# Optimization experiments

Hardware: AMD Instinct MI355X
Metric: run time of the kernel (lower is better)

Reference implementation:

```python
import jax, jax.numpy as jnp
import numpy as np

MAX_VALUATION = 5  # init kwarg
N = 4096           # == n_samples, so subsampling branch is skipped
D = 512
IDX_MAX = 200000


def setup_inputs() -> dict:
    key = jax.random.key(0)
    k1, k2 = jax.random.split(key)
    z = jax.random.normal(k1, (N, D), dtype=jnp.float32)
    indices = jax.random.randint(k2, (N,), 0, IDX_MAX, dtype=jnp.int64 if jax.config.jax_enable_x64 else jnp.int32)
    return {"z": z, "indices": indices}


def _pairwise_dist(z):
    # torch.cdist(z, z), p=2, with a sqrt-safe formulation
    sq = jnp.sum(z * z, axis=-1)                      # [n]
    d2 = sq[:, None] + sq[None, :] - 2.0 * (z @ z.T)  # [n, n]
    d2 = jnp.maximum(d2, 0.0)
    pos = d2 > 0.0
    return jnp.where(pos, jnp.sqrt(jnp.where(pos, d2, 1.0)), 0.0)


def _valuation_capped(diff, cap):
    # v3(diff) capped at `cap`: v >= t  <=>  diff % 3**t == 0 (for diff > 0)
    val = jnp.zeros(diff.shape, dtype=jnp.int32)
    for t in range(1, cap + 1):
        val = val + (diff % (3 ** t) == 0).astype(jnp.int32)
    return val


def reference(z, indices):
    n = z.shape[0]
    dist = _pairwise_dist(z)                               # [n, n]
    diff = jnp.abs(indices[:, None] - indices[None, :])    # [n, n] int
    # cap valuation at MAX_VALUATION+1 so over-cap pairs match no level v<=MAX_VALUATION
    val = _valuation_capped(diff, MAX_VALUATION + 1)
    upper = jnp.triu(jnp.ones((n, n), dtype=bool), k=1)
    valid = upper & (diff > 0)

    total = jnp.float32(0.0)
    level_count = jnp.float32(0.0)
    for v in range(MAX_VALUATION + 1):
        target = jnp.float32(3.0 ** (-v))
        weight = jnp.float32(1.0 / (v + 1))
        mask = valid & (val == v)
        cnt = jnp.sum(mask)
        sq = jnp.where(mask, (dist - target) ** 2, 0.0)
        mse = jnp.sum(sq) / jnp.maximum(cnt, 1).astype(jnp.float32)
        use = cnt >= 2  # original skips levels with <2 pairs
        total = total + jnp.where(use, weight * mse, 0.0)
        level_count = level_count + use.astype(jnp.float32)
    return total / jnp.maximum(level_count, 1.0)
```

## Files before the change

### kernel.cpp

```cpp
#include <hip/hip_runtime.h>
#include <hip/hip_bf16.h>
#include <stdint.h>

typedef unsigned short u16;
typedef unsigned int   u32;
typedef unsigned long long u64;

#define N_ROWS 4096
#define DIM    512
#define NT64   64
#define NPAIR64 2080
#define MOD3   729
#define NLEV   6
#define NKP    8
#define NSLOT  64

typedef __attribute__((ext_vector_type(2))) long  long2v;
typedef __attribute__((ext_vector_type(4))) float f32x4;

#define WS_ZPK 0
#define WS_SQ  (N_ROWS * DIM)
#define WS_R   (WS_SQ + N_ROWS * 4)
#define WS_ACC (WS_R + N_ROWS * 4)

__global__ __launch_bounds__(256)
void prep_kernel(const float* __restrict__ z, const int* __restrict__ idx,
                 u64* __restrict__ zpack, float* __restrict__ sq,
                 int* __restrict__ rres, u32* __restrict__ acczero)
{
    const int lane = threadIdx.x & 63;
    const int row  = blockIdx.x * 4 + (threadIdx.x >> 6);
    const float4* zr = reinterpret_cast<const float4*>(z + (size_t)row * DIM) + lane * 2;
    float4 v0 = zr[0], v1 = zr[1];
    float f[8] = {v0.x, v0.y, v0.z, v0.w, v1.x, v1.y, v1.z, v1.w};
    float ss = 0.f;
#pragma unroll
    for (int k = 0; k < 8; ++k) ss += f[k] * f[k];
    int lo = __builtin_amdgcn_cvt_pk_fp8_f32(f[0], f[1], 0, false);
    lo     = __builtin_amdgcn_cvt_pk_fp8_f32(f[2], f[3], lo, true);
    int hi = __builtin_amdgcn_cvt_pk_fp8_f32(f[4], f[5], 0, false);
    hi     = __builtin_amdgcn_cvt_pk_fp8_f32(f[6], f[7], hi, true);
    const u64 pk = (u64)(u32)lo | ((u64)(u32)hi << 32);
    zpack[((size_t)((row >> 4) * 8 + (lane >> 3)) << 7)
          + ((lane & 3) * 16 + (row & 15)) * 2 + ((lane >> 2) & 1)] = pk;
#pragma unroll
    for (int off = 32; off > 0; off >>= 1) ss += __shfl_down(ss, off, 64);
    if (lane == 0) {
        sq[row]   = ss;
        rres[row] = idx[row] % MOD3;
    }
    if (row == 0) {
#pragma unroll
        for (int i = 0; i < 16; ++i) acczero[lane + i * 64] = 0u;
    }
}

template<bool DIAG>
__device__ __forceinline__ void epilogue_acc(
    const f32x4 (&acc)[4][4], const float* sqI, const float* sqJ,
    const int* rI, const int* rJ, int lane,
    float (&lsum)[NLEV], u64& pcnt)
{
    const int rbase = (lane >> 4) * 4;
    const int cbase = lane & 15;
#pragma unroll
    for (int m = 0; m < 4; ++m) {
        const int il0 = m * 16 + rbase;
#pragma unroll
        for (int n = 0; n < 4; ++n) {
            const int jl  = n * 16 + cbase;
            const float sqj = sqJ[jl];
            const int   rj  = rJ[jl];
#pragma unroll
            for (int q = 0; q < 4; ++q) {
                const int il = il0 + q;
                float d2 = fmaxf(sqI[il] + sqj - 2.0f * acc[m][n][q], 0.f);
                const float dist = __builtin_amdgcn_sqrtf(d2);
                int dm = rI[il] - rj;
                dm += (dm >> 31) & MOD3;
                const u32 x = (u32)dm;
                int v =
                    (x * 2863311531u <= 1431655765u) +
                    (x *  954437177u <=  477218588u) +
                    (x * 1749801491u <=  159072862u) +
                    (x * 2014922929u <=   53024287u) +
                    (x * 3534952507u <=   17674762u) +
                    (x * 4041629033u <=    5891587u);
                if (DIAG) {
                    v = (jl > il) ? v : 6;
                }
                float tv = 1.0f;
                tv = (v == 1) ? (1.f / 3.f)   : tv;
                tv = (v == 2) ? (1.f / 9.f)   : tv;
                tv = (v == 3) ? (1.f / 27.f)  : tv;
                tv = (v == 4) ? (1.f / 81.f)  : tv;
                tv = (v == 5) ? (1.f / 243.f) : tv;
                const float dd  = dist - tv;
                const float sqd = dd * dd;
#pragma unroll
                for (int vv = 0; vv < NLEV; ++vv)
                    lsum[vv] += (v == vv) ? sqd : 0.f;
                pcnt += 1ull << (8 * v);
            }
        }
    }
}

__global__ __launch_bounds__(64, 2)
void pair_kernel(const u64* __restrict__ zpack, const float* __restrict__ sq,
                 const int* __restrict__ rres, float* __restrict__ gsum2,
                 u32* __restrict__ gcnt2)
{
    __shared__ __align__(16) u64 sb[2][8][128];
    __shared__ float sqI[64], sqJ[64];
    __shared__ int   rI[64], rJ[64];

    const int lane = threadIdx.x;

    const int wg = (blockIdx.x & 7) * (NPAIR64 / 8) + (blockIdx.x >> 3);
    int t = wg, ti = 0, rem = NT64;
    while (t >= rem) { t -= rem; ++ti; --rem; }
    const int tj = ti + t;
    const int I0 = ti * 64, J0 = tj * 64;

    __builtin_amdgcn_global_load_lds(
        (const __attribute__((address_space(1))) u32*)(sq + I0 + lane),
        (__attribute__((address_space(3))) u32*)sqI, 4, 0, 0);
    __builtin_amdgcn_global_load_lds(
        (const __attribute__((address_space(1))) u32*)(sq + J0 + lane),
        (__attribute__((address_space(3))) u32*)sqJ, 4, 0, 0);
    __builtin_amdgcn_global_load_lds(
        (const __attribute__((address_space(1))) u32*)(rres + I0 + lane),
        (__attribute__((address_space(3))) u32*)rI, 4, 0, 0);
    __builtin_amdgcn_global_load_lds(
        (const __attribute__((address_space(1))) u32*)(rres + J0 + lane),
        (__attribute__((address_space(3))) u32*)rJ, 4, 0, 0);

    const int RA = ti * 4, RB = tj * 4;

#define STAGE(buf, kp)                                                         \
    {                                                                          \
        _Pragma("unroll")                                                      \
        for (int g = 0; g < 4; ++g) {                                          \
            __builtin_amdgcn_global_load_lds(                                  \
                (const __attribute__((address_space(1))) u32*)                 \
                    (zpack + (((size_t)(RA + g) * 8 + (kp)) << 7) + lane * 2), \
                (__attribute__((address_space(3))) u32*)&sb[buf][g][0],        \
                16, 0, 0);                                                     \
            __builtin_amdgcn_global_load_lds(                                  \
                (const __attribute__((address_space(1))) u32*)                 \
                    (zpack + (((size_t)(RB + g) * 8 + (kp)) << 7) + lane * 2), \
                (__attribute__((address_space(3))) u32*)&sb[buf][4 + g][0],    \
                16, 0, 0);                                                     \
        }                                                                      \
    }

    f32x4 acc[4][4];
#pragma unroll
    for (int m = 0; m < 4; ++m)
#pragma unroll
        for (int n = 0; n < 4; ++n) acc[m][n] = (f32x4){0.f, 0.f, 0.f, 0.f};

    STAGE(0, 0);
#pragma unroll
    for (int kp = 0; kp < NKP; ++kp) {
        const int buf = kp & 1;
        if (kp + 1 < NKP) {
            STAGE(buf ^ 1, kp + 1);
            asm volatile("s_waitcnt vmcnt(8)" ::: "memory");
        } else {
            asm volatile("s_waitcnt vmcnt(0)" ::: "memory");
        }
        __builtin_amdgcn_sched_barrier(0);
        long2v A[4], B[4];
#pragma unroll
        for (int g = 0; g < 4; ++g) {
            A[g] = reinterpret_cast<const long2v*>(&sb[buf][g][0])[lane];
            B[g] = reinterpret_cast<const long2v*>(&sb[buf][4 + g][0])[lane];
        }
#pragma unroll
        for (int h = 0; h < 2; ++h)
#pragma unroll
            for (int m = 0; m < 4; ++m)
#pragma unroll
                for (int n = 0; n < 4; ++n)
                    acc[m][n] = __builtin_amdgcn_mfma_f32_16x16x32_fp8_fp8(
                        A[m][h], B[n][h], acc[m][n], 0, 0, 0);
    }
#undef STAGE

    float lsum[NLEV] = {0.f, 0.f, 0.f, 0.f, 0.f, 0.f};
    u64 pcnt = 0ull;
    if (ti == tj) epilogue_acc<true >(acc, sqI, sqJ, rI, rJ, lane, lsum, pcnt);
    else          epilogue_acc<false>(acc, sqI, sqJ, rI, rJ, lane, lsum, pcnt);

    const int slot = (int)(blockIdx.x & (NSLOT - 1));
#pragma unroll
    for (int vv = 0; vv < NLEV; ++vv) {
        float s = lsum[vv];
        u32   c = (u32)((pcnt >> (8 * vv)) & 255ull);
#pragma unroll
        for (int off = 32; off > 0; off >>= 1) {
            s += __shfl_xor(s, off, 64);
            c += __shfl_xor(c, off, 64);
        }
        if (lane == 0) {
            atomicAdd(&gsum2[slot * 8 + vv], s);
            atomicAdd(&gcnt2[slot * 8 + vv], c);
        }
    }
}

__global__ __launch_bounds__(64)
void finalize_kernel(const float* __restrict__ gsum2,
                     const u32* __restrict__ gcnt2,
                     float* __restrict__ out)
{
    const int lane = threadIdx.x;
    float s[NLEV];
    u32   c[NLEV];
#pragma unroll
    for (int v = 0; v < NLEV; ++v) {
        s[v] = gsum2[lane * 8 + v];
        c[v] = gcnt2[lane * 8 + v];
    }
#pragma unroll
    for (int v = 0; v < NLEV; ++v) {
#pragma unroll
        for (int off = 32; off > 0; off >>= 1) {
            s[v] += __shfl_xor(s[v], off, 64);
            c[v] += __shfl_xor(c[v], off, 64);
        }
    }
    if (lane == 0) {
        const float w[NLEV] = {1.f, 1.f / 2.f, 1.f / 3.f, 1.f / 4.f, 1.f / 5.f, 1.f / 6.f};
        float total = 0.f, lc = 0.f;
#pragma unroll
        for (int v = 0; v < NLEV; ++v) {
            const float cnt = (float)c[v];
            const float mse = s[v] / fmaxf(cnt, 1.f);
            const bool  use = c[v] >= 2u;
            total += use ? w[v] * mse : 0.f;
            lc    += use ? 1.f : 0.f;
        }
        out[0] = total / fmaxf(lc, 1.f);
    }
}

extern "C" void kernel_launch(void* const* d_in, const int* in_sizes, int n_in,
                              void* d_out, int out_size, void* d_ws, size_t ws_size,
                              hipStream_t stream)
{
    const float* z   = (const float*)d_in[0];
    const int*   idx = (const int*)d_in[1];
    char* ws = (char*)d_ws;
    u64*   zpk   = (u64*)(ws + WS_ZPK);
    float* sq    = (float*)(ws + WS_SQ);
    int*   rres  = (int*)(ws + WS_R);
    float* gsum2 = (float*)(ws + WS_ACC);
    u32*   gcnt2 = (u32*)(ws + WS_ACC + NSLOT * 8 * 4);
    float* out   = (float*)d_out;

    prep_kernel<<<N_ROWS / 4, 256, 0, stream>>>(z, idx, zpk, sq, rres, (u32*)gsum2);
    pair_kernel<<<NPAIR64, 64, 0, stream>>>(zpk, sq, rres, gsum2, gcnt2);
    finalize_kernel<<<1, 64, 0, stream>>>(gsum2, gcnt2, out);
}
```

Baseline: 37.39 us.

## Precompute per-level counts via residue histogram and use LUT weights in pair epilogue

A histogram of index residues mod 729 now gives the per-level pair counts in closed form. The per-level MSE weights are folded into a 729-entry coefficient/target lookup table, so the pair kernel accumulates a single weighted sum per pair instead of six sums plus packed counts. The pair tile also shrinks from 64x64 to 32x32, which gives four times as many workgroups and higher occupancy. The cost is an extra memset and a single-block count kernel, more redundant operand loads across smaller tiles, and LDS lookups with data-dependent addresses.

```diff
diff --git a/kernel.cpp b/kernel.cpp
--- a/kernel.cpp
+++ b/kernel.cpp
@@ -8,25 +8,29 @@
 
 #define N_ROWS 4096
 #define DIM    512
-#define NT64   64
-#define NPAIR64 2080
+#define NT32   128
+#define NPAIR32 8256
 #define MOD3   729
-#define NLEV   6
 #define NKP    8
 #define NSLOT  64
 
 typedef __attribute__((ext_vector_type(2))) long  long2v;
+typedef __attribute__((ext_vector_type(2))) float f32x2;
 typedef __attribute__((ext_vector_type(4))) float f32x4;
 
-#define WS_ZPK 0
-#define WS_SQ  (N_ROWS * DIM)
-#define WS_R   (WS_SQ + N_ROWS * 4)
-#define WS_ACC (WS_R + N_ROWS * 4)
+#define WS_ZPK  0
+#define WS_SQ   (N_ROWS * DIM)
+#define WS_R    (WS_SQ + N_ROWS * 4)
+#define WS_HIST (WS_R + N_ROWS * 4)
+#define WS_GS   (WS_HIST + 736 * 4)
+#define WS_META (WS_GS + 64 * 4)
+#define WS_LUTG (WS_META + 16)
+#define WS_ZERO_BYTES (736 * 4 + 64 * 4)
 
 __global__ __launch_bounds__(256)
 void prep_kernel(const float* __restrict__ z, const int* __restrict__ idx,
                  u64* __restrict__ zpack, float* __restrict__ sq,
-                 int* __restrict__ rres, u32* __restrict__ acczero)
+                 int* __restrict__ rres, u32* __restrict__ hist)
 {
     const int lane = threadIdx.x & 63;
     const int row  = blockIdx.x * 4 + (threadIdx.x >> 6);
@@ -46,102 +50,143 @@
 #pragma unroll
     for (int off = 32; off > 0; off >>= 1) ss += __shfl_down(ss, off, 64);
     if (lane == 0) {
-        sq[row]   = ss;
-        rres[row] = idx[row] % MOD3;
-    }
-    if (row == 0) {
-#pragma unroll
-        for (int i = 0; i < 16; ++i) acczero[lane + i * 64] = 0u;
+        sq[row] = ss;
+        const int r = idx[row] % MOD3;
+        rres[row] = r;
+        atomicAdd(&hist[r], 1u);
+    }
+}
+
+__global__ __launch_bounds__(768)
+void count_kernel(const u32* __restrict__ hist, float* __restrict__ lutg,
+                  float* __restrict__ meta)
+{
+    __shared__ u32 h[736];
+    __shared__ u32 T[8];
+    __shared__ float cf[8];
+    const int tid = threadIdx.x;
+    if (tid < 736) h[tid] = (tid < 729) ? hist[tid] : 0u;
+    if (tid < 8)   T[tid] = 0u;
+    __syncthreads();
+    if (tid < 729) { u32 x = h[tid]; if (x > 1) atomicAdd(&T[6], x * (x - 1) / 2u); }
+    __syncthreads();
+    if (tid < 243) h[tid] = h[tid] + h[tid + 243] + h[tid + 486];
+    __syncthreads();
+    if (tid < 243) { u32 x = h[tid]; if (x > 1) atomicAdd(&T[5], x * (x - 1) / 2u); }
+    __syncthreads();
+    if (tid < 81) h[tid] = h[tid] + h[tid + 81] + h[tid + 162];
+    __syncthreads();
+    if (tid < 81) { u32 x = h[tid]; if (x > 1) atomicAdd(&T[4], x * (x - 1) / 2u); }
+    __syncthreads();
+    if (tid < 27) h[tid] = h[tid] + h[tid + 27] + h[tid + 54];
+    __syncthreads();
+    if (tid < 27) { u32 x = h[tid]; if (x > 1) atomicAdd(&T[3], x * (x - 1) / 2u); }
+    __syncthreads();
+    if (tid < 9) h[tid] = h[tid] + h[tid + 9] + h[tid + 18];
+    __syncthreads();
+    if (tid < 9) { u32 x = h[tid]; if (x > 1) atomicAdd(&T[2], x * (x - 1) / 2u); }
+    __syncthreads();
+    if (tid < 3) h[tid] = h[tid] + h[tid + 3] + h[tid + 6];
+    __syncthreads();
+    if (tid < 3) { u32 x = h[tid]; if (x > 1) atomicAdd(&T[1], x * (x - 1) / 2u); }
+    __syncthreads();
+    if (tid == 0) {
+        u32 cnt[6];
+        cnt[0] = (u32)((u64)N_ROWS * (N_ROWS - 1) / 2) - T[1];
+        cnt[1] = T[1] - T[2]; cnt[2] = T[2] - T[3]; cnt[3] = T[3] - T[4];
+        cnt[4] = T[4] - T[5]; cnt[5] = T[5] - T[6];
+        const float w[6] = {1.f, 0.5f, 1.f / 3.f, 0.25f, 0.2f, 1.f / 6.f};
+        float lc = 0.f;
+#pragma unroll
+        for (int v = 0; v < 6; ++v) {
+            const bool use = cnt[v] >= 2u;
+            cf[v] = use ? w[v] / (float)cnt[v] : 0.f;
+            lc += use ? 1.f : 0.f;
+        }
+        cf[6] = 0.f; cf[7] = 0.f;
+        meta[0] = (lc > 0.f) ? lc : 1.f;
+    }
+    __syncthreads();
+    {
+        const int e = tid;
+        float coef = 0.f, tv = 0.f;
+        if (e < 729) {
+            int v = 6;
+            if (e != 0) { v = 0; int y = e; while (v < 6 && y % 3 == 0) { y /= 3; ++v; } }
+            const float tvs[7] = {1.f, 1.f / 3.f, 1.f / 9.f, 1.f / 27.f,
+                                  1.f / 81.f, 1.f / 243.f, 0.f};
+            coef = cf[v];
+            tv   = tvs[v];
+        }
+        lutg[2 * e]     = coef;
+        lutg[2 * e + 1] = tv;
     }
 }
 
 template<bool DIAG>
 __device__ __forceinline__ void epilogue_acc(
-    const f32x4 (&acc)[4][4], const float* sqI, const float* sqJ,
-    const int* rI, const int* rJ, int lane,
-    float (&lsum)[NLEV], u64& pcnt)
+    const f32x4 (&acc)[2][2], const float* sqIJ, const int* rIJ,
+    const float* lut, int lane, float& S)
 {
     const int rbase = (lane >> 4) * 4;
     const int cbase = lane & 15;
 #pragma unroll
-    for (int m = 0; m < 4; ++m) {
-        const int il0 = m * 16 + rbase;
-#pragma unroll
-        for (int n = 0; n < 4; ++n) {
-            const int jl  = n * 16 + cbase;
-            const float sqj = sqJ[jl];
-            const int   rj  = rJ[jl];
+    for (int m = 0; m < 2; ++m)
+#pragma unroll
+        for (int n = 0; n < 2; ++n)
 #pragma unroll
             for (int q = 0; q < 4; ++q) {
-                const int il = il0 + q;
-                float d2 = fmaxf(sqI[il] + sqj - 2.0f * acc[m][n][q], 0.f);
+                const int il = m * 16 + rbase + q;
+                const int jl = n * 16 + cbase;
+                float d2 = fmaxf(sqIJ[il] + sqIJ[32 + jl] - 2.0f * acc[m][n][q], 0.f);
                 const float dist = __builtin_amdgcn_sqrtf(d2);
-                int dm = rI[il] - rj;
+                int dm = rIJ[il] - rIJ[32 + jl];
                 dm += (dm >> 31) & MOD3;
-                const u32 x = (u32)dm;
-                int v =
-                    (x * 2863311531u <= 1431655765u) +
-                    (x *  954437177u <=  477218588u) +
-                    (x * 1749801491u <=  159072862u) +
-                    (x * 2014922929u <=   53024287u) +
-                    (x * 3534952507u <=   17674762u) +
-                    (x * 4041629033u <=    5891587u);
-                if (DIAG) {
-                    v = (jl > il) ? v : 6;
-                }
-                float tv = 1.0f;
-                tv = (v == 1) ? (1.f / 3.f)   : tv;
-                tv = (v == 2) ? (1.f / 9.f)   : tv;
-                tv = (v == 3) ? (1.f / 27.f)  : tv;
-                tv = (v == 4) ? (1.f / 81.f)  : tv;
-                tv = (v == 5) ? (1.f / 243.f) : tv;
-                const float dd  = dist - tv;
-                const float sqd = dd * dd;
-#pragma unroll
-                for (int vv = 0; vv < NLEV; ++vv)
-                    lsum[vv] += (v == vv) ? sqd : 0.f;
-                pcnt += 1ull << (8 * v);
+                const f32x2 ct = *reinterpret_cast<const f32x2*>(&lut[dm * 2]);
+                float coef = ct[0];
+                if (DIAG) coef = (jl > il) ? coef : 0.f;
+                const float dd = dist - ct[1];
+                S += coef * dd * dd;
             }
-        }
-    }
-}
-
-__global__ __launch_bounds__(64, 2)
+}
+
+__global__ __launch_bounds__(64, 4)
 void pair_kernel(const u64* __restrict__ zpack, const float* __restrict__ sq,
-                 const int* __restrict__ rres, float* __restrict__ gsum2,
-                 u32* __restrict__ gcnt2)
-{
-    __shared__ __align__(16) u64 sb[2][8][128];
-    __shared__ float sqI[64], sqJ[64];
-    __shared__ int   rI[64], rJ[64];
+                 const int* __restrict__ rres, const float* __restrict__ lutg,
+                 float* __restrict__ gS)
+{
+    __shared__ __align__(16) u64   sb[2][4][128];
+    __shared__ __align__(16) float lut[1536];
+    __shared__ __align__(16) float sqIJ[64];
+    __shared__ __align__(16) int   rIJ[64];
 
     const int lane = threadIdx.x;
 
-    const int wg = (blockIdx.x & 7) * (NPAIR64 / 8) + (blockIdx.x >> 3);
-    int t = wg, ti = 0, rem = NT64;
+    const int wg = (blockIdx.x & 7) * (NPAIR32 / 8) + (blockIdx.x >> 3);
+    int t = wg, ti = 0, rem = NT32;
     while (t >= rem) { t -= rem; ++ti; --rem; }
     const int tj = ti + t;
-    const int I0 = ti * 64, J0 = tj * 64;
-
+    const int I0 = ti * 32, J0 = tj * 32;
+
+    const int gsrc = (lane < 32) ? (I0 + lane) : (J0 + lane - 32);
     __builtin_amdgcn_global_load_lds(
-        (const __attribute__((address_space(1))) u32*)(sq + I0 + lane),
-        (__attribute__((address_space(3))) u32*)sqI, 4, 0, 0);
+        (const __attribute__((address_space(1))) u32*)(sq + gsrc),
+        (__attribute__((address_space(3))) u32*)sqIJ, 4, 0, 0);
     __builtin_amdgcn_global_load_lds(
-        (const __attribute__((address_space(1))) u32*)(sq + J0 + lane),
-        (__attribute__((address_space(3))) u32*)sqJ, 4, 0, 0);
-    __builtin_amdgcn_global_load_lds(
-        (const __attribute__((address_space(1))) u32*)(rres + I0 + lane),
-        (__attribute__((address_space(3))) u32*)rI, 4, 0, 0);
-    __builtin_amdgcn_global_load_lds(
-        (const __attribute__((address_space(1))) u32*)(rres + J0 + lane),
-        (__attribute__((address_space(3))) u32*)rJ, 4, 0, 0);
-
-    const int RA = ti * 4, RB = tj * 4;
+        (const __attribute__((address_space(1))) u32*)(rres + gsrc),
+        (__attribute__((address_space(3))) u32*)rIJ, 4, 0, 0);
+#pragma unroll
+    for (int i = 0; i < 6; ++i)
+        __builtin_amdgcn_global_load_lds(
+            (const __attribute__((address_space(1))) u32*)(lutg + i * 256 + lane * 4),
+            (__attribute__((address_space(3))) u32*)&lut[i * 256], 16, 0, 0);
+
+    const int RA = 2 * ti, RB = 2 * tj;
 
 #define STAGE(buf, kp)                                                         \
     {                                                                          \
         _Pragma("unroll")                                                      \
-        for (int g = 0; g < 4; ++g) {                                          \
+        for (int g = 0; g < 2; ++g) {                                          \
             __builtin_amdgcn_global_load_lds(                                  \
                 (const __attribute__((address_space(1))) u32*)                 \
                     (zpack + (((size_t)(RA + g) * 8 + (kp)) << 7) + lane * 2), \
@@ -150,16 +195,16 @@
             __builtin_amdgcn_global_load_lds(                                  \
                 (const __attribute__((address_space(1))) u32*)                 \
                     (zpack + (((size_t)(RB + g) * 8 + (kp)) << 7) + lane * 2), \
-                (__attribute__((address_space(3))) u32*)&sb[buf][4 + g][0],    \
+                (__attribute__((address_space(3))) u32*)&sb[buf][2 + g][0],    \
                 16, 0, 0);                                                     \
         }                                                                      \
     }
 
-    f32x4 acc[4][4];
-#pragma unroll
-    for (int m = 0; m < 4; ++m)
-#pragma unroll
-        for (int n = 0; n < 4; ++n) acc[m][n] = (f32x4){0.f, 0.f, 0.f, 0.f};
+    f32x4 acc[2][2];
+#pragma unroll
+    for (int m = 0; m < 2; ++m)
+#pragma unroll
+        for (int n = 0; n < 2; ++n) acc[m][n] = (f32x4){0.f, 0.f, 0.f, 0.f};
 
     STAGE(0, 0);
 #pragma unroll
@@ -167,84 +212,46 @@
         const int buf = kp & 1;
         if (kp + 1 < NKP) {
             STAGE(buf ^ 1, kp + 1);
-            asm volatile("s_waitcnt vmcnt(8)" ::: "memory");
+            asm volatile("s_waitcnt vmcnt(4)" ::: "memory");
         } else {
             asm volatile("s_waitcnt vmcnt(0)" ::: "memory");
         }
         __builtin_amdgcn_sched_barrier(0);
-        long2v A[4], B[4];
-#pragma unroll
-        for (int g = 0; g < 4; ++g) {
+        long2v A[2], B[2];
+#pragma unroll
+        for (int g = 0; g < 2; ++g) {
             A[g] = reinterpret_cast<const long2v*>(&sb[buf][g][0])[lane];
-            B[g] = reinterpret_cast<const long2v*>(&sb[buf][4 + g][0])[lane];
+            B[g] = reinterpret_cast<const long2v*>(&sb[buf][2 + g][0])[lane];
         }
 #pragma unroll
         for (int h = 0; h < 2; ++h)
 #pragma unroll
-            for (int m = 0; m < 4; ++m)
-#pragma unroll
-                for (int n = 0; n < 4; ++n)
+            for (int m = 0; m < 2; ++m)
+#pragma unroll
+                for (int n = 0; n < 2; ++n)
                     acc[m][n] = __builtin_amdgcn_mfma_f32_16x16x32_fp8_fp8(
                         A[m][h], B[n][h], acc[m][n], 0, 0, 0);
     }
 #undef STAGE
 
-    float lsum[NLEV] = {0.f, 0.f, 0.f, 0.f, 0.f, 0.f};
-    u64 pcnt = 0ull;
-    if (ti == tj) epilogue_acc<true >(acc, sqI, sqJ, rI, rJ, lane, lsum, pcnt);
-    else          epilogue_acc<false>(acc, sqI, sqJ, rI, rJ, lane, lsum, pcnt);
-
-    const int slot = (int)(blockIdx.x & (NSLOT - 1));
-#pragma unroll
-    for (int vv = 0; vv < NLEV; ++vv) {
-        float s = lsum[vv];
-        u32   c = (u32)((pcnt >> (8 * vv)) & 255ull);
-#pragma unroll
-        for (int off = 32; off > 0; off >>= 1) {
-            s += __shfl_xor(s, off, 64);
-            c += __shfl_xor(c, off, 64);
-        }
-        if (lane == 0) {
-            atomicAdd(&gsum2[slot * 8 + vv], s);
-            atomicAdd(&gcnt2[slot * 8 + vv], c);
-        }
-    }
+    float S = 0.f;
+    if (ti == tj) epilogue_acc<true >(acc, sqIJ, rIJ, lut, lane, S);
+    else          epilogue_acc<false>(acc, sqIJ, rIJ, lut, lane, S);
+
+#pragma unroll
+    for (int off = 32; off > 0; off >>= 1) S += __shfl_xor(S, off, 64);
+    if (lane == 0) atomicAdd(&gS[blockIdx.x & (NSLOT - 1)], S);
 }
 
 __global__ __launch_bounds__(64)
-void finalize_kernel(const float* __restrict__ gsum2,
-                     const u32* __restrict__ gcnt2,
-                     float* __restrict__ out)
+void finalize_kernel(const float* __restrict__ gS,
+                     const float* __restrict__ meta, float* __restrict__ out)
 {
     const int lane = threadIdx.x;
-    float s[NLEV];
-    u32   c[NLEV];
-#pragma unroll
-    for (int v = 0; v < NLEV; ++v) {
-        s[v] = gsum2[lane * 8 + v];
-        c[v] = gcnt2[lane * 8 + v];
-    }
-#pragma unroll
-    for (int v = 0; v < NLEV; ++v) {
-#pragma unroll
-        for (int off = 32; off > 0; off >>= 1) {
-            s[v] += __shfl_xor(s[v], off, 64);
-            c[v] += __shfl_xor(c[v], off, 64);
-        }
-    }
-    if (lane == 0) {
-        const float w[NLEV] = {1.f, 1.f / 2.f, 1.f / 3.f, 1.f / 4.f, 1.f / 5.f, 1.f / 6.f};
-        float total = 0.f, lc = 0.f;
-#pragma unroll
-        for (int v = 0; v < NLEV; ++v) {
-            const float cnt = (float)c[v];
-            const float mse = s[v] / fmaxf(cnt, 1.f);
-            const bool  use = c[v] >= 2u;
-            total += use ? w[v] * mse : 0.f;
-            lc    += use ? 1.f : 0.f;
-        }
-        out[0] = total / fmaxf(lc, 1.f);
-    }
+    float s = gS[lane];
+#pragma unroll
+    for (int off = 32; off > 0; off >>= 1) s += __shfl_xor(s, off, 64);
+    if (lane == 0) out[0] = s / meta[0];
 }
 
 extern "C" void kernel_launch(void* const* d_in, const int* in_sizes, int n_in,
@@ -254,14 +261,18 @@
     const float* z   = (const float*)d_in[0];
     const int*   idx = (const int*)d_in[1];
     char* ws = (char*)d_ws;
-    u64*   zpk   = (u64*)(ws + WS_ZPK);
-    float* sq    = (float*)(ws + WS_SQ);
-    int*   rres  = (int*)(ws + WS_R);
-    float* gsum2 = (float*)(ws + WS_ACC);
-    u32*   gcnt2 = (u32*)(ws + WS_ACC + NSLOT * 8 * 4);
-    float* out   = (float*)d_out;
-
-    prep_kernel<<<N_ROWS / 4, 256, 0, stream>>>(z, idx, zpk, sq, rres, (u32*)gsum2);
-    pair_kernel<<<NPAIR64, 64, 0, stream>>>(zpk, sq, rres, gsum2, gcnt2);
-    finalize_kernel<<<1, 64, 0, stream>>>(gsum2, gcnt2, out);
-}
+    u64*   zpk  = (u64*)(ws + WS_ZPK);
+    float* sq   = (float*)(ws + WS_SQ);
+    int*   rres = (int*)(ws + WS_R);
+    u32*   hist = (u32*)(ws + WS_HIST);
+    float* gS   = (float*)(ws + WS_GS);
+    float* meta = (float*)(ws + WS_META);
+    float* lutg = (float*)(ws + WS_LUTG);
+    float* out  = (float*)d_out;
+
+    hipMemsetAsync(ws + WS_HIST, 0, WS_ZERO_BYTES, stream);
+    prep_kernel<<<N_ROWS / 4, 256, 0, stream>>>(z, idx, zpk, sq, rres, hist);
+    count_kernel<<<1, 768, 0, stream>>>(hist, lutg, meta);
+    pair_kernel<<<NPAIR32, 64, 0, stream>>>(zpk, sq, rres, lutg, gS);
+    finalize_kernel<<<1, 64, 0, stream>>>(gS, meta, out);
+}
```

New measurement: 62.91 us. 68.2% more time.
